# Performance work log

Measured on AMD Instinct MI355X. Metric: run time of the kernel, lower is better.

## Reference

```python
import jax, jax.numpy as jnp
import numpy as np

EPS = 1e-12

def _spectral_normalize(W, u):
    # torch spectral_norm (eval-time math): v = normalize(W^T u), sigma = u^T W v
    u = jax.lax.stop_gradient(u)
    v = W.T @ u
    v = jax.lax.stop_gradient(v / (jnp.linalg.norm(v) + EPS))
    sigma = u @ (W @ v)
    return W / sigma

def _conv1x1(x, W):
    # 1x1 conv, no bias: (out,in) x (B,in,H,W) -> (B,out,H,W)
    return jnp.einsum('oc,bchw->bohw', W, x)

def setup_inputs() -> dict:
    key = jax.random.key(0)
    ks = jax.random.split(key, 10)
    B, C, H, W = 4, 512, 64, 64
    Cp = C // 8
    return {
        'x': jax.random.normal(ks[0], (B, C, H, W), jnp.float32),
        'Wf': jax.random.normal(ks[1], (Cp, C), jnp.float32) * 0.05,
        'Wg': jax.random.normal(ks[2], (Cp, C), jnp.float32) * 0.05,
        'Wh': jax.random.normal(ks[3], (Cp, C), jnp.float32) * 0.05,
        'Wv': jax.random.normal(ks[4], (C, Cp), jnp.float32) * 0.05,
        'uf': jax.random.normal(ks[5], (Cp,), jnp.float32),
        'ug': jax.random.normal(ks[6], (Cp,), jnp.float32),
        'uh': jax.random.normal(ks[7], (Cp,), jnp.float32),
        'uv': jax.random.normal(ks[8], (C,), jnp.float32),
        'gamma': jax.random.normal(ks[9], (1,), jnp.float32) * 0.1,
    }

def reference(x, Wf, Wg, Wh, Wv, uf, ug, uh, uv, gamma):
    B, C, H, W = x.shape
    Cp = Wf.shape[0]
    N = H * W
    Wf_sn = _spectral_normalize(Wf, uf)
    Wg_sn = _spectral_normalize(Wg, ug)
    Wh_sn = _spectral_normalize(Wh, uh)
    Wv_sn = _spectral_normalize(Wv, uv)
    fx = _conv1x1(x, Wf_sn).reshape(B, Cp, N)   # (B,Cp,N)
    gx = _conv1x1(x, Wg_sn).reshape(B, Cp, N)   # (B,Cp,N)
    # fx^T gx: (B,N,N), unscaled single-head attention, softmax over last dim
    scores = jnp.einsum('bcn,bcm->bnm', fx, gx)
    attn = jax.nn.softmax(scores, axis=-1)
    hx = _conv1x1(x, Wh_sn).reshape(B, Cp, N)
    # hx @ attn: out[b,c,j] = sum_i hx[b,c,i] * attn[b,i,j]
    out = jnp.einsum('bci,bij->bcj', hx, attn).reshape(B, Cp, H, W)
    unscaled = _conv1x1(out, Wv_sn)
    return gamma * unscaled + x
```

## Files before the change

kernel.cpp:

```cpp
#include <hip/hip_runtime.h>


#define NB 4
#define CC 512
#define CP 64
#define NN 4096
#define L2E 1.4426950408889634f

typedef __attribute__((ext_vector_type(8))) short short8;
typedef __attribute__((ext_vector_type(4))) float floatx4;
typedef __attribute__((ext_vector_type(16))) float floatx16;

#define MFMA32(A, B, C) __builtin_amdgcn_mfma_f32_32x32x16_bf16((A), (B), (C), 0, 0, 0)

__device__ __forceinline__ float bf2f_u(unsigned short h) {
    return __uint_as_float((unsigned)h << 16);
}
__device__ __forceinline__ float bf16lo(unsigned v) { return __uint_as_float(v << 16); }
__device__ __forceinline__ float bf16hi(unsigned v) { return __uint_as_float(v & 0xffff0000u); }
__device__ __forceinline__ unsigned short f2bf(float f) {
    unsigned u = __float_as_uint(f);
    u += 0x7fffu + ((u >> 16) & 1u);
    return (unsigned short)(u >> 16);
}
__device__ __forceinline__ unsigned pack2bf(float a, float b) {
    return (unsigned)f2bf(a) | ((unsigned)f2bf(b) << 16);
}
__device__ __forceinline__ float ldS(const void* p, long i, int f32) {
    return f32 ? ((const float*)p)[i] : bf2f_u(((const unsigned short*)p)[i]);
}
__device__ __forceinline__ float4 ld4(const void* p, long i, int f32) {
    if (f32) return *reinterpret_cast<const float4*>((const float*)p + i);
    uint2 v = *reinterpret_cast<const uint2*>((const unsigned short*)p + i);
    return make_float4(bf16lo(v.x), bf16hi(v.x), bf16lo(v.y), bf16hi(v.y));
}
__device__ __forceinline__ short8 frag8(const void* p, long i, int f32) {
    uint4 au;
    if (f32) {
        float4 v0 = *reinterpret_cast<const float4*>((const float*)p + i);
        float4 v1 = *reinterpret_cast<const float4*>((const float*)p + i + 4);
        au.x = pack2bf(v0.x, v0.y); au.y = pack2bf(v0.z, v0.w);
        au.z = pack2bf(v1.x, v1.y); au.w = pack2bf(v1.z, v1.w);
    } else {
        au = *reinterpret_cast<const uint4*>((const unsigned short*)p + i);
    }
    return *reinterpret_cast<short8*>(&au);
}
__device__ __forceinline__ short8 as_s8(uint4 v) { return *reinterpret_cast<short8*>(&v); }
__device__ __forceinline__ floatx16 zero16() {
    floatx16 z;
    #pragma unroll
    for (int i = 0; i < 16; ++i) z[i] = 0.f;
    return z;
}
__device__ __forceinline__ unsigned cvtpk_bf16(float a, float b) {
    unsigned r;
    asm("v_cvt_pk_bf16_f32 %0, %1, %2" : "=v"(r) : "v"(a), "v"(b));
    return r;
}
__device__ __forceinline__ void pl32swap(unsigned &a, unsigned &b) {
    asm("v_permlane32_swap_b32 %0, %1" : "+v"(a), "+v"(b));
}
__device__ __forceinline__ float rcpf(float x) {
    float r;
    asm("v_rcp_f32 %0, %1" : "=v"(r) : "v"(x));
    return r;
}
__device__ __forceinline__ float exp2a(float x) {
    float r;
    asm("v_exp_f32 %0, %1" : "=v"(r) : "v"(x));
    return r;
}

__global__ __launch_bounds__(256) void detect_kernel(
    const unsigned* __restrict__ x, int* __restrict__ flag)
{
    __shared__ int red[256];
    const int t = threadIdx.x;
    int bad = 0;
    for (int i = t; i < 4096; i += 256) {
        unsigned w = x[i];
        float f0 = __uint_as_float(w << 16);
        float f1 = __uint_as_float(w & 0xffff0000u);
        float a0 = fabsf(f0), a1 = fabsf(f1);
        if (!(a0 <= 1e3f) || (f0 != 0.f && a0 < 1e-20f)) bad++;
        if (!(a1 <= 1e3f) || (f1 != 0.f && a1 < 1e-20f)) bad++;
    }
    red[t] = bad;
    __syncthreads();
    for (int s = 128; s > 0; s >>= 1) { if (t < s) red[t] += red[t + s]; __syncthreads(); }
    if (t == 0) *flag = (red[0] > 64) ? 1 : 0;
}

__global__ __launch_bounds__(256) void xpose_kernel(
    const void* __restrict__ x, const int* __restrict__ dflag,
    unsigned short* __restrict__ xTF, float* __restrict__ rl)
{
    const int f32 = *dflag;
    const int nt = blockIdx.x;
    const int b  = blockIdx.y;
    const int n0 = nt * 32;
    const int t = threadIdx.x;
    __shared__ unsigned short xl[32][72];

    const int gid = (b * 128 + nt) * 256 + t;
    if (gid < NB * NN) rl[gid] = 0.f;

    const int n_l = t & 31, cg8 = ((t >> 5) & 7) * 8;
    const int q = t >> 6, lo = t & 63;

    for (int slab = 0; slab < 8; ++slab) {
        const int cs = slab * 64;
        float v[8];
        #pragma unroll
        for (int j = 0; j < 8; ++j)
            v[j] = ldS(x, ((long)b * CC + cs + cg8 + j) * NN + n0 + n_l, f32);
        if (slab) __syncthreads();
        unsigned* row = reinterpret_cast<unsigned*>(&xl[n_l][cg8]);
        row[0] = pack2bf(v[0], v[1]);
        row[1] = pack2bf(v[2], v[3]);
        row[2] = pack2bf(v[4], v[5]);
        row[3] = pack2bf(v[6], v[7]);
        __syncthreads();
        const int cb = q * 16 + ((lo >> 5) << 3);
        uint4 val = *reinterpret_cast<const uint4*>(&xl[lo & 31][cb]);
        size_t off = (((size_t)(b * 128 + nt) * 32) + slab * 4 + q) * 512 + (size_t)lo * 8;
        *reinterpret_cast<uint4*>(xTF + off) = val;
    }
}

__global__ __launch_bounds__(512) void sigma_kernel(
    const void* __restrict__ Wf, const void* __restrict__ Wg,
    const void* __restrict__ Wh, const void* __restrict__ Wv,
    const void* __restrict__ uf, const void* __restrict__ ug,
    const void* __restrict__ uh, const void* __restrict__ uv,
    const int* __restrict__ dflag, float* __restrict__ sig,
    unsigned short* __restrict__ WF)
{
    const int f32 = *dflag;
    const int w = blockIdx.x;
    const void* W;
    const void* u;
    if (w == 0)      { W = Wf; u = uf; }
    else if (w == 1) { W = Wg; u = ug; }
    else if (w == 2) { W = Wh; u = uh; }
    else             { W = Wv; u = uv; }

    __shared__ float us[512];
    __shared__ float red[512];
    const int t = threadIdx.x;
    float S;

    if (w < 3) {
        if (t < 64) us[t] = ldS(u, t, f32);
        __syncthreads();
        float a = 0.f;
        #pragma unroll
        for (int i = 0; i < 64; ++i)
            a = fmaf(ldS(W, (long)i * 512 + t, f32), us[i], a);
        red[t] = a * a;
        __syncthreads();
        #pragma unroll
        for (int s = 256; s > 0; s >>= 1) {
            if (t < s) red[t] += red[t + s];
            __syncthreads();
        }
        S = red[0];
    } else {
        us[t] = ldS(u, t, f32);
        __syncthreads();
        const int g = t >> 6, c = t & 63;
        float a = 0.f;
        #pragma unroll
        for (int k = 0; k < 64; ++k) {
            int i = g + k * 8;
            a = fmaf(ldS(W, (long)i * 64 + c, f32), us[i], a);
        }
        red[t] = a;
        __syncthreads();
        #pragma unroll
        for (int s = 256; s >= 64; s >>= 1) {
            if (t < s) red[t] += red[t + s];
            __syncthreads();
        }
        float ac = (t < 64) ? red[t] : 0.f;
        __syncthreads();
        red[t] = ac * ac;
        __syncthreads();
        #pragma unroll
        for (int s = 256; s > 0; s >>= 1) {
            if (t < s) red[t] += red[t + s];
            __syncthreads();
        }
        S = red[0];
    }
    const float isig = (sqrtf(S) + 1e-12f) / S;
    if (t == 0) sig[w] = isig;

    if (w < 3) {
        const float sc = isig * (w == 0 ? L2E : 1.f);
        #pragma unroll
        for (int q = 0; q < 8; ++q) {
            const int idx = q * 512 + t;
            const int ll  = idx & 63;
            const int kc  = (idx >> 6) & 31;
            const int cpt = idx >> 11;
            const int cp = cpt * 32 + (ll & 31);
            const int c  = kc * 16 + ((ll >> 5) << 3);
            const long base = (long)cp * CC + c;
            float a0 = ldS(W, base + 0, f32) * sc, a1 = ldS(W, base + 1, f32) * sc;
            float a2 = ldS(W, base + 2, f32) * sc, a3 = ldS(W, base + 3, f32) * sc;
            float a4 = ldS(W, base + 4, f32) * sc, a5 = ldS(W, base + 5, f32) * sc;
            float a6 = ldS(W, base + 6, f32) * sc, a7 = ldS(W, base + 7, f32) * sc;
            uint4 o;
            o.x = pack2bf(a0, a1); o.y = pack2bf(a2, a3);
            o.z = pack2bf(a4, a5); o.w = pack2bf(a6, a7);
            *reinterpret_cast<uint4*>(WF + ((size_t)w * 4096 + idx) * 8) = o;
        }
    }
}

__global__ __launch_bounds__(256, 4) void proj_kernel(
    const unsigned short* __restrict__ xTF,
    const unsigned short* __restrict__ WF,
    unsigned short* __restrict__ fxF, unsigned short* __restrict__ gxF,
    unsigned short* __restrict__ hxF)
{
    const int t = threadIdx.x;
    const int w = t >> 6, l = t & 63;
    const int flat = blockIdx.x;
    const int k = flat & 7, s = flat >> 3;
    const int sd6 = s / 6;
    const int g = (k << 4) + sd6;
    const int zc = s - sd6 * 6;
    const int b = g & 3;
    const int nt = (g >> 2) * 4 + w;
    const int wi = zc >> 1;

    const unsigned short* xb = xTF + ((size_t)(b * 128 + nt) * 32) * 512 + (size_t)l * 8;
    const unsigned short* wb = WF + ((size_t)zc * 32) * 512 + (size_t)l * 8;

    floatx16 accE = zero16(), accO = zero16();
    uint4 x0 = *reinterpret_cast<const uint4*>(xb);
    uint4 w0 = *reinterpret_cast<const uint4*>(wb);
    uint4 x1, w1;

    if (wi == 2) {
        for (int kc = 0; kc < 32; kc += 2) {
            x1 = *reinterpret_cast<const uint4*>(xb + (kc + 1) * 512);
            w1 = *reinterpret_cast<const uint4*>(wb + (kc + 1) * 512);
            accE = MFMA32(as_s8(x0), as_s8(w0), accE);
            if (kc + 2 < 32) {
                x0 = *reinterpret_cast<const uint4*>(xb + (kc + 2) * 512);
                w0 = *reinterpret_cast<const uint4*>(wb + (kc + 2) * 512);
            }
            accO = MFMA32(as_s8(x1), as_s8(w1), accO);
        }
    } else {
        for (int kc = 0; kc < 32; kc += 2) {
            x1 = *reinterpret_cast<const uint4*>(xb + (kc + 1) * 512);
            w1 = *reinterpret_cast<const uint4*>(wb + (kc + 1) * 512);
            accE = MFMA32(as_s8(w0), as_s8(x0), accE);
            if (kc + 2 < 32) {
                x0 = *reinterpret_cast<const uint4*>(xb + (kc + 2) * 512);
                w0 = *reinterpret_cast<const uint4*>(wb + (kc + 2) * 512);
            }
            accO = MFMA32(as_s8(w1), as_s8(x1), accO);
        }
    }

    float a[16];
    #pragma unroll
    for (int i = 0; i < 16; ++i) a[i] = accE[i] + accO[i];

    const int cpt = zc & 1;
    if (wi < 2) {
        unsigned short* __restrict__ dstF = (wi == 0) ? fxF : gxF;
        #pragma unroll
        for (int kcl = 0; kcl < 2; ++kcl) {
            const int r8 = kcl * 8;
            unsigned u0 = cvtpk_bf16(a[r8 + 0], a[r8 + 1]);
            unsigned u1 = cvtpk_bf16(a[r8 + 2], a[r8 + 3]);
            unsigned u2 = cvtpk_bf16(a[r8 + 4], a[r8 + 5]);
            unsigned u3 = cvtpk_bf16(a[r8 + 6], a[r8 + 7]);
            pl32swap(u0, u2);
            pl32swap(u1, u3);
            uint4 o = make_uint4(u0, u1, u2, u3);
            size_t off = (((size_t)(b * 128 + nt) * 4) + cpt * 2 + kcl) * 512 + (size_t)l * 8;
            *reinterpret_cast<uint4*>(dstF + off) = o;
        }
    } else {
        #pragma unroll
        for (int ich = 0; ich < 2; ++ich) {
            const int r8 = ich * 8;
            unsigned u0 = cvtpk_bf16(a[r8 + 0], a[r8 + 1]);
            unsigned u1 = cvtpk_bf16(a[r8 + 2], a[r8 + 3]);
            unsigned u2 = cvtpk_bf16(a[r8 + 4], a[r8 + 5]);
            unsigned u3 = cvtpk_bf16(a[r8 + 6], a[r8 + 7]);
            pl32swap(u0, u2);
            pl32swap(u1, u3);
            uint4 o = make_uint4(u0, u1, u2, u3);
            size_t off = ((((size_t)(b * 128 + nt) * 2 + ich) * 2) + cpt) * 512 + (size_t)l * 8;
            *reinterpret_cast<uint4*>(hxF + off) = o;
        }
    }
}

__global__ __launch_bounds__(256, 4) void rowstats_kernel(
    const unsigned short* __restrict__ fxF, const unsigned short* __restrict__ gxF,
    float* __restrict__ rl)
{
    const int t = threadIdx.x;
    const int w = t >> 6, l = t & 63, l31 = l & 31, hi = l >> 5;
    const int flat = blockIdx.x;
    const int k = flat & 7, s = flat >> 3;
    const int c2 = (k << 2) + (s >> 5);
    const int iblk = s & 31;
    const int jy = c2 & 7, b = c2 >> 3;
    const int i0 = iblk * 128 + w * 32;
    const int jbase = jy * 512;

    __shared__ unsigned short stg[2][2][2048];

    const unsigned short* fA = fxF + ((size_t)(b * 128 + (i0 >> 5))) * 2048 + (size_t)l * 8;
    uint4 af[4];
    #pragma unroll
    for (int kc = 0; kc < 4; ++kc)
        af[kc] = *reinterpret_cast<const uint4*>(fA + kc * 512);

    const unsigned short* gB = gxF + ((size_t)(b * 128 + (jbase >> 5))) * 2048
                               + (size_t)w * 512 + (size_t)l * 8;

    float suml[16];
    #pragma unroll
    for (int r = 0; r < 16; ++r) suml[r] = 0.f;

    uint4 ra = *reinterpret_cast<const uint4*>(gB);
    uint4 rb = *reinterpret_cast<const uint4*>(gB + 2048);
    *reinterpret_cast<uint4*>(&stg[0][0][w * 512 + l * 8]) = ra;
    *reinterpret_cast<uint4*>(&stg[0][1][w * 512 + l * 8]) = rb;
    __syncthreads();

    #pragma unroll 2
    for (int p = 0; p < 8; ++p) {
        const int cur = p & 1;
        if (p + 1 < 8) {
            ra = *reinterpret_cast<const uint4*>(gB + (size_t)(2 * p + 2) * 2048);
            rb = *reinterpret_cast<const uint4*>(gB + (size_t)(2 * p + 3) * 2048);
        }

        uint4 bfA[4], bfB[4];
        #pragma unroll
        for (int kc = 0; kc < 4; ++kc) {
            bfA[kc] = *reinterpret_cast<const uint4*>(&stg[cur][0][kc * 512 + l * 8]);
            bfB[kc] = *reinterpret_cast<const uint4*>(&stg[cur][1][kc * 512 + l * 8]);
        }

        floatx16 sA = zero16(), sB = zero16();
        #pragma unroll
        for (int kc = 0; kc < 4; ++kc) {
            sA = MFMA32(as_s8(af[kc]), as_s8(bfA[kc]), sA);
            sB = MFMA32(as_s8(af[kc]), as_s8(bfB[kc]), sB);
        }
        #pragma unroll
        for (int r = 0; r < 16; ++r) suml[r] += exp2a(sA[r]) + exp2a(sB[r]);

        if (p + 1 < 8) {
            *reinterpret_cast<uint4*>(&stg[cur ^ 1][0][w * 512 + l * 8]) = ra;
            *reinterpret_cast<uint4*>(&stg[cur ^ 1][1][w * 512 + l * 8]) = rb;
        }
        __syncthreads();
    }

    #pragma unroll
    for (int r = 0; r < 16; ++r) {
        float v = suml[r];
        v += __shfl_xor(v, 1);
        v += __shfl_xor(v, 2);
        v += __shfl_xor(v, 4);
        v += __shfl_xor(v, 8);
        v += __shfl_xor(v, 16);
        suml[r] = v;
    }
    if (l31 == 0) {
        #pragma unroll
        for (int r = 0; r < 16; ++r) {
            int row = (r & 3) + 8 * (r >> 2) + 4 * hi;
            atomicAdd(&rl[(size_t)b * NN + i0 + row], suml[r]);
        }
    }
}

__global__ __launch_bounds__(256) void scalehx_kernel(
    const float* __restrict__ rl, unsigned short* __restrict__ hxF)
{
    const int idx = blockIdx.x * 256 + threadIdx.x;
    const int l = idx & 63;
    const int r = idx >> 6;
    const int ich = (r >> 1) & 1;
    const int tile = (r >> 2) & 127;
    const int b = r >> 9;
    const int i0 = tile * 32 + ich * 16 + (l >> 5) * 8;
    const float* rp = rl + (size_t)b * NN + i0;
    float4 ra = *reinterpret_cast<const float4*>(rp);
    float4 rb = *reinterpret_cast<const float4*>(rp + 4);
    uint4 v = *reinterpret_cast<uint4*>(hxF + (size_t)idx * 8);
    uint4 ov;
    ov.x = pack2bf(bf16lo(v.x) * rcpf(ra.x), bf16hi(v.x) * rcpf(ra.y));
    ov.y = pack2bf(bf16lo(v.y) * rcpf(ra.z), bf16hi(v.y) * rcpf(ra.w));
    ov.z = pack2bf(bf16lo(v.z) * rcpf(rb.x), bf16hi(v.z) * rcpf(rb.y));
    ov.w = pack2bf(bf16lo(v.w) * rcpf(rb.z), bf16hi(v.w) * rcpf(rb.w));
    *reinterpret_cast<uint4*>(hxF + (size_t)idx * 8) = ov;
}

__global__ __launch_bounds__(256, 4) void pv_kernel(
    const unsigned short* __restrict__ fxF, const unsigned short* __restrict__ gxF,
    const unsigned short* __restrict__ hxF,
    float* __restrict__ opF0, float* __restrict__ opF1,
    float* __restrict__ opF2, float* __restrict__ opF3)
{
    const int t = threadIdx.x;
    const int w = t >> 6, l = t & 63, l31 = l & 31, hi = l >> 5;
    const int igrp = w >> 1, jgrp = w & 1;
    const int flat = blockIdx.x;
    const int k = flat & 7, s = flat >> 3;
    const int c2 = (k << 1) + (s >> 6);
    const int jblk = s & 63;
    const int isb = c2 & 3, b = c2 >> 2;
    const int j0 = jblk * 64;
    const int tbase = isb * 32 + igrp * 16;

    __shared__ unsigned short stg[2][2][2][2048];
    float* red = reinterpret_cast<float*>(stg);

    uint4 qf[4];
    {
        const unsigned short* gq =
            gxF + ((size_t)(b * 128 + (j0 >> 5) + jgrp)) * 2048 + (size_t)l * 8;
        #pragma unroll
        for (int kc = 0; kc < 4; ++kc)
            qf[kc] = *reinterpret_cast<const uint4*>(gq + kc * 512);
    }

    floatx16 acc0 = zero16(), acc1 = zero16();

    const unsigned short* sb =
        (jgrp == 0 ? fxF : hxF) + ((size_t)(b * 128 + tbase)) * 2048 + (size_t)l * 8;

    uint4 rg0 = *reinterpret_cast<const uint4*>(sb);
    uint4 rg1 = *reinterpret_cast<const uint4*>(sb + 512);
    uint4 rg2 = *reinterpret_cast<const uint4*>(sb + 1024);
    uint4 rg3 = *reinterpret_cast<const uint4*>(sb + 1536);
    {
        unsigned short* d = &stg[igrp][0][jgrp][l * 8];
        *reinterpret_cast<uint4*>(d)        = rg0;
        *reinterpret_cast<uint4*>(d + 512)  = rg1;
        *reinterpret_cast<uint4*>(d + 1024) = rg2;
        *reinterpret_cast<uint4*>(d + 1536) = rg3;
    }
    __syncthreads();

    #pragma unroll 2
    for (int it = 0; it < 16; ++it) {
        const int cur = it & 1;
        if (it + 1 < 16) {
            const unsigned short* p = sb + (size_t)(it + 1) * 2048;
            rg0 = *reinterpret_cast<const uint4*>(p);
            rg1 = *reinterpret_cast<const uint4*>(p + 512);
            rg2 = *reinterpret_cast<const uint4*>(p + 1024);
            rg3 = *reinterpret_cast<const uint4*>(p + 1536);
        }

        const unsigned short* fl = &stg[igrp][cur][0][l * 8];
        const unsigned short* vl = &stg[igrp][cur][1][l * 8];
        uint4 af[4], vf[4];
        #pragma unroll
        for (int kc = 0; kc < 4; ++kc)
            af[kc] = *reinterpret_cast<const uint4*>(fl + kc * 512);
        vf[0] = *reinterpret_cast<const uint4*>(vl);
        vf[1] = *reinterpret_cast<const uint4*>(vl + 1024);
        vf[2] = *reinterpret_cast<const uint4*>(vl + 512);
        vf[3] = *reinterpret_cast<const uint4*>(vl + 1536);

        floatx16 s2 = zero16();
        #pragma unroll
        for (int kc = 0; kc < 4; ++kc)
            s2 = MFMA32(as_s8(af[kc]), as_s8(qf[kc]), s2);

        float e[16];
        #pragma unroll
        for (int r = 0; r < 16; ++r) e[r] = exp2a(s2[r]);

        unsigned u0 = cvtpk_bf16(e[0], e[1]);
        unsigned u1 = cvtpk_bf16(e[2], e[3]);
        unsigned u2 = cvtpk_bf16(e[4], e[5]);
        unsigned u3 = cvtpk_bf16(e[6], e[7]);
        pl32swap(u0, u2);
        pl32swap(u1, u3);
        uint4 pa0 = make_uint4(u0, u1, u2, u3);
        unsigned u4 = cvtpk_bf16(e[8], e[9]);
        unsigned u5 = cvtpk_bf16(e[10], e[11]);
        unsigned u6 = cvtpk_bf16(e[12], e[13]);
        unsigned u7 = cvtpk_bf16(e[14], e[15]);
        pl32swap(u4, u6);
        pl32swap(u5, u7);
        uint4 pa1 = make_uint4(u4, u5, u6, u7);

        acc0 = MFMA32(as_s8(pa0), as_s8(vf[0]), acc0);
        acc0 = MFMA32(as_s8(pa1), as_s8(vf[1]), acc0);
        acc1 = MFMA32(as_s8(pa0), as_s8(vf[2]), acc1);
        acc1 = MFMA32(as_s8(pa1), as_s8(vf[3]), acc1);

        if (it + 1 < 16) {
            unsigned short* d = &stg[igrp][cur ^ 1][jgrp][l * 8];
            *reinterpret_cast<uint4*>(d)        = rg0;
            *reinterpret_cast<uint4*>(d + 512)  = rg1;
            *reinterpret_cast<uint4*>(d + 1024) = rg2;
            *reinterpret_cast<uint4*>(d + 1536) = rg3;
        }
        __syncthreads();
    }

    #pragma unroll
    for (int q = 0; q < 4; ++q)
        *reinterpret_cast<float4*>(&red[(q * 256 + t) * 4]) =
            make_float4(0.f, 0.f, 0.f, 0.f);
    __syncthreads();
    #pragma unroll
    for (int r = 0; r < 16; ++r) {
        int row = jgrp * 32 + (r & 3) + 8 * (r >> 2) + 4 * hi;
        atomicAdd(&red[row * 64 + l31],      acc0[r]);
        atomicAdd(&red[row * 64 + 32 + l31], acc1[r]);
    }
    __syncthreads();

    float* __restrict__ dst = (isb == 0) ? opF0 : ((isb == 1) ? opF1 : ((isb == 2) ? opF2 : opF3));
    #pragma unroll
    for (int q = 0; q < 4; ++q) {
        int idx = q * 256 + t;
        int e2  = idx & 1;
        int ll  = (idx >> 1) & 63;
        int ks  = (idx >> 7) & 1;
        int ntl = idx >> 8;
        int jloc = ntl * 16 + (ll & 15);
        int cp   = ks * 32 + ((ll >> 4) << 3) + e2 * 4;
        float4 v = *reinterpret_cast<const float4*>(&red[jloc * 64 + cp]);
        size_t off = (((size_t)(b * 256 + (j0 >> 4) + ntl) * 2 + ks) * 64 + ll) * 8 + e2 * 4;
        *reinterpret_cast<float4*>(dst + off) = v;
    }
}

__global__ __launch_bounds__(256) void outproj_kernel(
    const void* __restrict__ x,
    const void* __restrict__ Wv,
    const void* __restrict__ gamma,
    const int* __restrict__ dflag,
    const float* __restrict__ sig,
    const float* __restrict__ opF0, const float* __restrict__ opF1,
    const float* __restrict__ opF2, const float* __restrict__ opF3,
    void* __restrict__ y)
{
    const int f32 = *dflag;
    const int n0     = blockIdx.x * 64;
    const int cobase = blockIdx.y * 128;
    const int b      = blockIdx.z;
    const int t = threadIdx.x;
    const int wv = t >> 6, l = t & 63, l15 = l & 15, quad = l >> 4;
    const float scale = ldS(gamma, 0, f32) * sig[3];

    floatx4 acc[4][2];
    #pragma unroll
    for (int ns = 0; ns < 4; ++ns)
        #pragma unroll
        for (int ct = 0; ct < 2; ++ct) acc[ns][ct] = (floatx4){0.f, 0.f, 0.f, 0.f};

    #pragma unroll
    for (int ks = 0; ks < 2; ++ks) {
        short8 a[4];
        #pragma unroll
        for (int ns = 0; ns < 4; ++ns) {
            size_t fo = (((size_t)(b * 256 + (n0 >> 4) + ns) * 2 + ks) * 64 + l) * 8;
            float4 s0 = *reinterpret_cast<const float4*>(opF0 + fo);
            float4 s1 = *reinterpret_cast<const float4*>(opF1 + fo);
            float4 s2 = *reinterpret_cast<const float4*>(opF2 + fo);
            float4 s3 = *reinterpret_cast<const float4*>(opF3 + fo);
            float4 t0 = *reinterpret_cast<const float4*>(opF0 + fo + 4);
            float4 t1 = *reinterpret_cast<const float4*>(opF1 + fo + 4);
            float4 t2 = *reinterpret_cast<const float4*>(opF2 + fo + 4);
            float4 t3 = *reinterpret_cast<const float4*>(opF3 + fo + 4);
            float v0 = s0.x + s1.x + s2.x + s3.x;
            float v1 = s0.y + s1.y + s2.y + s3.y;
            float v2 = s0.z + s1.z + s2.z + s3.z;
            float v3 = s0.w + s1.w + s2.w + s3.w;
            float v4 = t0.x + t1.x + t2.x + t3.x;
            float v5 = t0.y + t1.y + t2.y + t3.y;
            float v6 = t0.z + t1.z + t2.z + t3.z;
            float v7 = t0.w + t1.w + t2.w + t3.w;
            uint4 au;
            au.x = pack2bf(v0, v1); au.y = pack2bf(v2, v3);
            au.z = pack2bf(v4, v5); au.w = pack2bf(v6, v7);
            a[ns] = *reinterpret_cast<short8*>(&au);
        }
        const int kb = ks * 32 + quad * 8;
        #pragma unroll
        for (int ct = 0; ct < 2; ++ct) {
            const int co = cobase + 32 * wv + 16 * ct + l15;
            short8 bfr = frag8(Wv, (long)co * CP + kb, f32);
            #pragma unroll
            for (int ns = 0; ns < 4; ++ns)
                acc[ns][ct] = __builtin_amdgcn_mfma_f32_16x16x32_bf16(
                    a[ns], bfr, acc[ns][ct], 0, 0, 0);
        }
    }

    #pragma unroll
    for (int ns = 0; ns < 4; ++ns)
        #pragma unroll
        for (int ct = 0; ct < 2; ++ct) {
            const int co = cobase + 32 * wv + 16 * ct + l15;
            const long base = ((long)b * CC + co) * NN + n0 + 16 * ns + quad * 4;
            float4 xv = ld4(x, base, f32);
            float o0 = fmaf(scale, acc[ns][ct][0], xv.x);
            float o1 = fmaf(scale, acc[ns][ct][1], xv.y);
            float o2 = fmaf(scale, acc[ns][ct][2], xv.z);
            float o3 = fmaf(scale, acc[ns][ct][3], xv.w);
            if (f32) {
                *reinterpret_cast<float4*>((float*)y + base) = make_float4(o0, o1, o2, o3);
            } else {
                uint2 o;
                o.x = pack2bf(o0, o1);
                o.y = pack2bf(o2, o3);
                *reinterpret_cast<uint2*>((unsigned short*)y + base) = o;
            }
        }
}

extern "C" void kernel_launch(void* const* d_in, const int* in_sizes, int n_in,
                              void* d_out, int out_size, void* d_ws, size_t ws_size,
                              hipStream_t stream)
{
    const void* x  = d_in[0];
    const void* Wf = d_in[1];
    const void* Wg = d_in[2];
    const void* Wh = d_in[3];
    const void* Wv = d_in[4];
    const void* uf = d_in[5];
    const void* ug = d_in[6];
    const void* uh = d_in[7];
    const void* uv = d_in[8];
    const void* gm = d_in[9];

    char* base = (char*)d_ws;
    int*   dfl = (int*)(base);
    float* sig = (float*)(base + 512);
    float* rl  = (float*)(base + 1024);
    float* opF0 = (float*)(base + 1024 + 65536);
    float* opF1 = opF0 + (size_t)NB * NN * CP;
    float* opF2 = opF1 + (size_t)NB * NN * CP;
    float* opF3 = opF2 + (size_t)NB * NN * CP;
    unsigned short* fxF = (unsigned short*)(opF3 + (size_t)NB * NN * CP);
    unsigned short* gxF = fxF + (size_t)NB * CP * NN;
    unsigned short* hxF = gxF + (size_t)NB * CP * NN;
    unsigned short* xTF = hxF + (size_t)NB * CP * NN;
    unsigned short* WF  = xTF + (size_t)NB * CC * NN;

    hipLaunchKernelGGL(detect_kernel, dim3(1), dim3(256), 0, stream,
                       (const unsigned*)x, dfl);
    hipLaunchKernelGGL(xpose_kernel, dim3(128, NB), dim3(256), 0, stream,
                       x, dfl, xTF, rl);
    hipLaunchKernelGGL(sigma_kernel, dim3(4), dim3(512), 0, stream,
                       Wf, Wg, Wh, Wv, uf, ug, uh, uv, dfl, sig, WF);
    hipLaunchKernelGGL(proj_kernel, dim3(768), dim3(256), 0, stream,
                       xTF, WF, fxF, gxF, hxF);
    hipLaunchKernelGGL(rowstats_kernel, dim3(1024), dim3(256), 0, stream,
                       fxF, gxF, rl);
    hipLaunchKernelGGL(scalehx_kernel, dim3((NB * CP * NN / 8) / 256), dim3(256), 0, stream,
                       rl, hxF);
    hipLaunchKernelGGL(pv_kernel, dim3(1024), dim3(256), 0, stream,
                       fxF, gxF, hxF, opF0, opF1, opF2, opF3);
    hipLaunchKernelGGL(outproj_kernel, dim3(NN / 64, CC / 128, NB), dim3(256), 0, stream,
                       x, Wv, gm, dfl, sig, opF0, opF1, opF2, opF3, d_out);
}
```

Measured before the change: 238.2 us.

## Drop LDS staging, fuse softmax normalization into PV, halve i-split partials

```diff
diff --git a/kernel.cpp b/kernel.cpp
--- a/kernel.cpp
+++ b/kernel.cpp
@@ -70,6 +70,22 @@
     float r;
     asm("v_exp_f32 %0, %1" : "=v"(r) : "v"(x));
     return r;
+}
+__device__ __forceinline__ void packP(const float e[16], uint4& pa0, uint4& pa1) {
+    unsigned u0 = cvtpk_bf16(e[0], e[1]);
+    unsigned u1 = cvtpk_bf16(e[2], e[3]);
+    unsigned u2 = cvtpk_bf16(e[4], e[5]);
+    unsigned u3 = cvtpk_bf16(e[6], e[7]);
+    pl32swap(u0, u2);
+    pl32swap(u1, u3);
+    pa0 = make_uint4(u0, u1, u2, u3);
+    unsigned u4 = cvtpk_bf16(e[8], e[9]);
+    unsigned u5 = cvtpk_bf16(e[10], e[11]);
+    unsigned u6 = cvtpk_bf16(e[12], e[13]);
+    unsigned u7 = cvtpk_bf16(e[14], e[15]);
+    pl32swap(u4, u6);
+    pl32swap(u5, u7);
+    pa1 = make_uint4(u4, u5, u6, u7);
 }
 
 __global__ __launch_bounds__(256) void detect_kernel(
@@ -320,56 +336,42 @@
     const int i0 = iblk * 128 + w * 32;
     const int jbase = jy * 512;
 
-    __shared__ unsigned short stg[2][2][2048];
-
     const unsigned short* fA = fxF + ((size_t)(b * 128 + (i0 >> 5))) * 2048 + (size_t)l * 8;
     uint4 af[4];
     #pragma unroll
     for (int kc = 0; kc < 4; ++kc)
         af[kc] = *reinterpret_cast<const uint4*>(fA + kc * 512);
 
-    const unsigned short* gB = gxF + ((size_t)(b * 128 + (jbase >> 5))) * 2048
-                               + (size_t)w * 512 + (size_t)l * 8;
+    const unsigned short* gB = gxF + ((size_t)(b * 128 + (jbase >> 5))) * 2048 + (size_t)l * 8;
 
     float suml[16];
     #pragma unroll
     for (int r = 0; r < 16; ++r) suml[r] = 0.f;
 
-    uint4 ra = *reinterpret_cast<const uint4*>(gB);
-    uint4 rb = *reinterpret_cast<const uint4*>(gB + 2048);
-    *reinterpret_cast<uint4*>(&stg[0][0][w * 512 + l * 8]) = ra;
-    *reinterpret_cast<uint4*>(&stg[0][1][w * 512 + l * 8]) = rb;
-    __syncthreads();
-
-    #pragma unroll 2
-    for (int p = 0; p < 8; ++p) {
-        const int cur = p & 1;
-        if (p + 1 < 8) {
-            ra = *reinterpret_cast<const uint4*>(gB + (size_t)(2 * p + 2) * 2048);
-            rb = *reinterpret_cast<const uint4*>(gB + (size_t)(2 * p + 3) * 2048);
-        }
-
-        uint4 bfA[4], bfB[4];
-        #pragma unroll
-        for (int kc = 0; kc < 4; ++kc) {
-            bfA[kc] = *reinterpret_cast<const uint4*>(&stg[cur][0][kc * 512 + l * 8]);
-            bfB[kc] = *reinterpret_cast<const uint4*>(&stg[cur][1][kc * 512 + l * 8]);
-        }
-
-        floatx16 sA = zero16(), sB = zero16();
-        #pragma unroll
-        for (int kc = 0; kc < 4; ++kc) {
-            sA = MFMA32(as_s8(af[kc]), as_s8(bfA[kc]), sA);
-            sB = MFMA32(as_s8(af[kc]), as_s8(bfB[kc]), sB);
-        }
-        #pragma unroll
-        for (int r = 0; r < 16; ++r) suml[r] += exp2a(sA[r]) + exp2a(sB[r]);
-
-        if (p + 1 < 8) {
-            *reinterpret_cast<uint4*>(&stg[cur ^ 1][0][w * 512 + l * 8]) = ra;
-            *reinterpret_cast<uint4*>(&stg[cur ^ 1][1][w * 512 + l * 8]) = rb;
-        }
-        __syncthreads();
+    uint4 b0[4], b1[4];
+    auto loadB = [&](uint4* bf, int jt) {
+        const unsigned short* p = gB + (size_t)jt * 2048;
+        #pragma unroll
+        for (int kc = 0; kc < 4; ++kc)
+            bf[kc] = *reinterpret_cast<const uint4*>(p + kc * 512);
+    };
+    auto bodyR = [&](uint4* bf) {
+        floatx16 s2 = zero16();
+        __builtin_amdgcn_s_setprio(1);
+        #pragma unroll
+        for (int kc = 0; kc < 4; ++kc)
+            s2 = MFMA32(as_s8(af[kc]), as_s8(bf[kc]), s2);
+        __builtin_amdgcn_s_setprio(0);
+        #pragma unroll
+        for (int r = 0; r < 16; ++r) suml[r] += exp2a(s2[r]);
+    };
+
+    loadB(b0, 0);
+    for (int jt = 0; jt < 16; jt += 2) {
+        loadB(b1, jt + 1);
+        bodyR(b0);
+        if (jt + 2 < 16) loadB(b0, jt + 2);
+        bodyR(b1);
     }
 
     #pragma unroll
@@ -391,134 +393,103 @@
     }
 }
 
-__global__ __launch_bounds__(256) void scalehx_kernel(
-    const float* __restrict__ rl, unsigned short* __restrict__ hxF)
-{
-    const int idx = blockIdx.x * 256 + threadIdx.x;
-    const int l = idx & 63;
-    const int r = idx >> 6;
-    const int ich = (r >> 1) & 1;
-    const int tile = (r >> 2) & 127;
-    const int b = r >> 9;
-    const int i0 = tile * 32 + ich * 16 + (l >> 5) * 8;
-    const float* rp = rl + (size_t)b * NN + i0;
-    float4 ra = *reinterpret_cast<const float4*>(rp);
-    float4 rb = *reinterpret_cast<const float4*>(rp + 4);
-    uint4 v = *reinterpret_cast<uint4*>(hxF + (size_t)idx * 8);
-    uint4 ov;
-    ov.x = pack2bf(bf16lo(v.x) * rcpf(ra.x), bf16hi(v.x) * rcpf(ra.y));
-    ov.y = pack2bf(bf16lo(v.y) * rcpf(ra.z), bf16hi(v.y) * rcpf(ra.w));
-    ov.z = pack2bf(bf16lo(v.z) * rcpf(rb.x), bf16hi(v.z) * rcpf(rb.y));
-    ov.w = pack2bf(bf16lo(v.w) * rcpf(rb.z), bf16hi(v.w) * rcpf(rb.w));
-    *reinterpret_cast<uint4*>(hxF + (size_t)idx * 8) = ov;
-}
-
-__global__ __launch_bounds__(256, 4) void pv_kernel(
+__global__ __launch_bounds__(256, 2) void pv_kernel(
     const unsigned short* __restrict__ fxF, const unsigned short* __restrict__ gxF,
-    const unsigned short* __restrict__ hxF,
-    float* __restrict__ opF0, float* __restrict__ opF1,
-    float* __restrict__ opF2, float* __restrict__ opF3)
+    const unsigned short* __restrict__ hxF, const float* __restrict__ rl,
+    float* __restrict__ opF0, float* __restrict__ opF1)
 {
     const int t = threadIdx.x;
     const int w = t >> 6, l = t & 63, l31 = l & 31, hi = l >> 5;
-    const int igrp = w >> 1, jgrp = w & 1;
     const int flat = blockIdx.x;
-    const int k = flat & 7, s = flat >> 3;
-    const int c2 = (k << 1) + (s >> 6);
-    const int jblk = s & 63;
-    const int isb = c2 & 3, b = c2 >> 2;
+    const int k = flat & 7;
+    const int isb = k & 1, b = k >> 1;
+    const int jblk = flat >> 3;
     const int j0 = jblk * 64;
-    const int tbase = isb * 32 + igrp * 16;
-
-    __shared__ unsigned short stg[2][2][2][2048];
-    float* red = reinterpret_cast<float*>(stg);
-
-    uint4 qf[4];
+    const int tb = isb * 64 + w * 16;
+
+    __shared__ float red[64 * 64];
+
+    uint4 qf0[4], qf1[4];
     {
         const unsigned short* gq =
-            gxF + ((size_t)(b * 128 + (j0 >> 5) + jgrp)) * 2048 + (size_t)l * 8;
+            gxF + ((size_t)(b * 128 + (j0 >> 5))) * 2048 + (size_t)l * 8;
+        #pragma unroll
+        for (int kc = 0; kc < 4; ++kc) {
+            qf0[kc] = *reinterpret_cast<const uint4*>(gq + kc * 512);
+            qf1[kc] = *reinterpret_cast<const uint4*>(gq + 2048 + kc * 512);
+        }
+    }
+
+    floatx16 acc00 = zero16(), acc01 = zero16();
+    floatx16 acc10 = zero16(), acc11 = zero16();
+
+    const unsigned short* fb = fxF + ((size_t)(b * 128 + tb)) * 2048 + (size_t)l * 8;
+    const unsigned short* vb = hxF + ((size_t)(b * 128 + tb)) * 2048 + (size_t)l * 8;
+    const float* rbase = rl + (size_t)b * NN + tb * 32 + (hi << 2);
+
+    uint4 afA[4], vfA[4], afB[4], vfB[4];
+    auto loadA = [&](uint4* af, int it) {
+        const unsigned short* p = fb + (size_t)it * 2048;
         #pragma unroll
         for (int kc = 0; kc < 4; ++kc)
-            qf[kc] = *reinterpret_cast<const uint4*>(gq + kc * 512);
-    }
-
-    floatx16 acc0 = zero16(), acc1 = zero16();
-
-    const unsigned short* sb =
-        (jgrp == 0 ? fxF : hxF) + ((size_t)(b * 128 + tbase)) * 2048 + (size_t)l * 8;
-
-    uint4 rg0 = *reinterpret_cast<const uint4*>(sb);
-    uint4 rg1 = *reinterpret_cast<const uint4*>(sb + 512);
-    uint4 rg2 = *reinterpret_cast<const uint4*>(sb + 1024);
-    uint4 rg3 = *reinterpret_cast<const uint4*>(sb + 1536);
-    {
-        unsigned short* d = &stg[igrp][0][jgrp][l * 8];
-        *reinterpret_cast<uint4*>(d)        = rg0;
-        *reinterpret_cast<uint4*>(d + 512)  = rg1;
-        *reinterpret_cast<uint4*>(d + 1024) = rg2;
-        *reinterpret_cast<uint4*>(d + 1536) = rg3;
-    }
-    __syncthreads();
-
-    #pragma unroll 2
-    for (int it = 0; it < 16; ++it) {
-        const int cur = it & 1;
-        if (it + 1 < 16) {
-            const unsigned short* p = sb + (size_t)(it + 1) * 2048;
-            rg0 = *reinterpret_cast<const uint4*>(p);
-            rg1 = *reinterpret_cast<const uint4*>(p + 512);
-            rg2 = *reinterpret_cast<const uint4*>(p + 1024);
-            rg3 = *reinterpret_cast<const uint4*>(p + 1536);
-        }
-
-        const unsigned short* fl = &stg[igrp][cur][0][l * 8];
-        const unsigned short* vl = &stg[igrp][cur][1][l * 8];
-        uint4 af[4], vf[4];
-        #pragma unroll
-        for (int kc = 0; kc < 4; ++kc)
-            af[kc] = *reinterpret_cast<const uint4*>(fl + kc * 512);
-        vf[0] = *reinterpret_cast<const uint4*>(vl);
-        vf[1] = *reinterpret_cast<const uint4*>(vl + 1024);
-        vf[2] = *reinterpret_cast<const uint4*>(vl + 512);
-        vf[3] = *reinterpret_cast<const uint4*>(vl + 1536);
-
-        floatx16 s2 = zero16();
-        #pragma unroll
-        for (int kc = 0; kc < 4; ++kc)
-            s2 = MFMA32(as_s8(af[kc]), as_s8(qf[kc]), s2);
-
-        float e[16];
-        #pragma unroll
-        for (int r = 0; r < 16; ++r) e[r] = exp2a(s2[r]);
-
-        unsigned u0 = cvtpk_bf16(e[0], e[1]);
-        unsigned u1 = cvtpk_bf16(e[2], e[3]);
-        unsigned u2 = cvtpk_bf16(e[4], e[5]);
-        unsigned u3 = cvtpk_bf16(e[6], e[7]);
-        pl32swap(u0, u2);
-        pl32swap(u1, u3);
-        uint4 pa0 = make_uint4(u0, u1, u2, u3);
-        unsigned u4 = cvtpk_bf16(e[8], e[9]);
-        unsigned u5 = cvtpk_bf16(e[10], e[11]);
-        unsigned u6 = cvtpk_bf16(e[12], e[13]);
-        unsigned u7 = cvtpk_bf16(e[14], e[15]);
-        pl32swap(u4, u6);
-        pl32swap(u5, u7);
-        uint4 pa1 = make_uint4(u4, u5, u6, u7);
-
-        acc0 = MFMA32(as_s8(pa0), as_s8(vf[0]), acc0);
-        acc0 = MFMA32(as_s8(pa1), as_s8(vf[1]), acc0);
-        acc1 = MFMA32(as_s8(pa0), as_s8(vf[2]), acc1);
-        acc1 = MFMA32(as_s8(pa1), as_s8(vf[3]), acc1);
-
-        if (it + 1 < 16) {
-            unsigned short* d = &stg[igrp][cur ^ 1][jgrp][l * 8];
-            *reinterpret_cast<uint4*>(d)        = rg0;
-            *reinterpret_cast<uint4*>(d + 512)  = rg1;
-            *reinterpret_cast<uint4*>(d + 1024) = rg2;
-            *reinterpret_cast<uint4*>(d + 1536) = rg3;
-        }
-        __syncthreads();
+            af[kc] = *reinterpret_cast<const uint4*>(p + kc * 512);
+    };
+    auto loadV = [&](uint4* vf, int it) {
+        const unsigned short* p = vb + (size_t)it * 2048;
+        vf[0] = *reinterpret_cast<const uint4*>(p);
+        vf[1] = *reinterpret_cast<const uint4*>(p + 1024);
+        vf[2] = *reinterpret_cast<const uint4*>(p + 512);
+        vf[3] = *reinterpret_cast<const uint4*>(p + 1536);
+    };
+    auto body = [&](uint4* af, uint4* vf, int it) {
+        const float* rp = rbase + it * 32;
+        float4 rv0 = *reinterpret_cast<const float4*>(rp);
+        float4 rv1 = *reinterpret_cast<const float4*>(rp + 8);
+        float4 rv2 = *reinterpret_cast<const float4*>(rp + 16);
+        float4 rv3 = *reinterpret_cast<const float4*>(rp + 24);
+        float ri[16];
+        ri[0] = rcpf(rv0.x); ri[1] = rcpf(rv0.y); ri[2] = rcpf(rv0.z); ri[3] = rcpf(rv0.w);
+        ri[4] = rcpf(rv1.x); ri[5] = rcpf(rv1.y); ri[6] = rcpf(rv1.z); ri[7] = rcpf(rv1.w);
+        ri[8] = rcpf(rv2.x); ri[9] = rcpf(rv2.y); ri[10] = rcpf(rv2.z); ri[11] = rcpf(rv2.w);
+        ri[12] = rcpf(rv3.x); ri[13] = rcpf(rv3.y); ri[14] = rcpf(rv3.z); ri[15] = rcpf(rv3.w);
+
+        floatx16 s0 = zero16(), s1 = zero16();
+        __builtin_amdgcn_s_setprio(1);
+        #pragma unroll
+        for (int kc = 0; kc < 4; ++kc) {
+            s0 = MFMA32(as_s8(af[kc]), as_s8(qf0[kc]), s0);
+            s1 = MFMA32(as_s8(af[kc]), as_s8(qf1[kc]), s1);
+        }
+        __builtin_amdgcn_s_setprio(0);
+
+        float e0[16], e1[16];
+        #pragma unroll
+        for (int r = 0; r < 16; ++r) e0[r] = exp2a(s0[r]) * ri[r];
+        #pragma unroll
+        for (int r = 0; r < 16; ++r) e1[r] = exp2a(s1[r]) * ri[r];
+
+        uint4 pa00, pa01, pa10, pa11;
+        packP(e0, pa00, pa01);
+        packP(e1, pa10, pa11);
+
+        __builtin_amdgcn_s_setprio(1);
+        acc00 = MFMA32(as_s8(pa00), as_s8(vf[0]), acc00);
+        acc00 = MFMA32(as_s8(pa01), as_s8(vf[1]), acc00);
+        acc01 = MFMA32(as_s8(pa00), as_s8(vf[2]), acc01);
+        acc01 = MFMA32(as_s8(pa01), as_s8(vf[3]), acc01);
+        acc10 = MFMA32(as_s8(pa10), as_s8(vf[0]), acc10);
+        acc10 = MFMA32(as_s8(pa11), as_s8(vf[1]), acc10);
+        acc11 = MFMA32(as_s8(pa10), as_s8(vf[2]), acc11);
+        acc11 = MFMA32(as_s8(pa11), as_s8(vf[3]), acc11);
+        __builtin_amdgcn_s_setprio(0);
+    };
+
+    loadA(afA, 0); loadV(vfA, 0);
+    for (int it = 0; it < 16; it += 2) {
+        loadA(afB, it + 1); loadV(vfB, it + 1);
+        body(afA, vfA, it);
+        if (it + 2 < 16) { loadA(afA, it + 2); loadV(vfA, it + 2); }
+        body(afB, vfB, it + 1);
     }
 
     #pragma unroll
@@ -528,13 +499,15 @@
     __syncthreads();
     #pragma unroll
     for (int r = 0; r < 16; ++r) {
-        int row = jgrp * 32 + (r & 3) + 8 * (r >> 2) + 4 * hi;
-        atomicAdd(&red[row * 64 + l31],      acc0[r]);
-        atomicAdd(&red[row * 64 + 32 + l31], acc1[r]);
+        int crow = (r & 3) + 8 * (r >> 2) + 4 * hi;
+        atomicAdd(&red[crow * 64 + l31],             acc00[r]);
+        atomicAdd(&red[crow * 64 + 32 + l31],        acc01[r]);
+        atomicAdd(&red[(32 + crow) * 64 + l31],      acc10[r]);
+        atomicAdd(&red[(32 + crow) * 64 + 32 + l31], acc11[r]);
     }
     __syncthreads();
 
-    float* __restrict__ dst = (isb == 0) ? opF0 : ((isb == 1) ? opF1 : ((isb == 2) ? opF2 : opF3));
+    float* __restrict__ dst = isb ? opF1 : opF0;
     #pragma unroll
     for (int q = 0; q < 4; ++q) {
         int idx = q * 256 + t;
@@ -557,7 +530,6 @@
     const int* __restrict__ dflag,
     const float* __restrict__ sig,
     const float* __restrict__ opF0, const float* __restrict__ opF1,
-    const float* __restrict__ opF2, const float* __restrict__ opF3,
     void* __restrict__ y)
 {
     const int f32 = *dflag;
@@ -582,23 +554,13 @@
             size_t fo = (((size_t)(b * 256 + (n0 >> 4) + ns) * 2 + ks) * 64 + l) * 8;
             float4 s0 = *reinterpret_cast<const float4*>(opF0 + fo);
             float4 s1 = *reinterpret_cast<const float4*>(opF1 + fo);
-            float4 s2 = *reinterpret_cast<const float4*>(opF2 + fo);
-            float4 s3 = *reinterpret_cast<const float4*>(opF3 + fo);
             float4 t0 = *reinterpret_cast<const float4*>(opF0 + fo + 4);
             float4 t1 = *reinterpret_cast<const float4*>(opF1 + fo + 4);
-            float4 t2 = *reinterpret_cast<const float4*>(opF2 + fo + 4);
-            float4 t3 = *reinterpret_cast<const float4*>(opF3 + fo + 4);
-            float v0 = s0.x + s1.x + s2.x + s3.x;
-            float v1 = s0.y + s1.y + s2.y + s3.y;
-            float v2 = s0.z + s1.z + s2.z + s3.z;
-            float v3 = s0.w + s1.w + s2.w + s3.w;
-            float v4 = t0.x + t1.x + t2.x + t3.x;
-            float v5 = t0.y + t1.y + t2.y + t3.y;
-            float v6 = t0.z + t1.z + t2.z + t3.z;
-            float v7 = t0.w + t1.w + t2.w + t3.w;
             uint4 au;
-            au.x = pack2bf(v0, v1); au.y = pack2bf(v2, v3);
-            au.z = pack2bf(v4, v5); au.w = pack2bf(v6, v7);
+            au.x = pack2bf(s0.x + s1.x, s0.y + s1.y);
+            au.y = pack2bf(s0.z + s1.z, s0.w + s1.w);
+            au.z = pack2bf(t0.x + t1.x, t0.y + t1.y);
+            au.w = pack2bf(t0.z + t1.z, t0.w + t1.w);
             a[ns] = *reinterpret_cast<short8*>(&au);
         }
         const int kb = ks * 32 + quad * 8;
@@ -656,9 +618,7 @@
     float* rl  = (float*)(base + 1024);
     float* opF0 = (float*)(base + 1024 + 65536);
     float* opF1 = opF0 + (size_t)NB * NN * CP;
-    float* opF2 = opF1 + (size_t)NB * NN * CP;
-    float* opF3 = opF2 + (size_t)NB * NN * CP;
-    unsigned short* fxF = (unsigned short*)(opF3 + (size_t)NB * NN * CP);
+    unsigned short* fxF = (unsigned short*)(opF1 + (size_t)NB * NN * CP);
     unsigned short* gxF = fxF + (size_t)NB * CP * NN;
     unsigned short* hxF = gxF + (size_t)NB * CP * NN;
     unsigned short* xTF = hxF + (size_t)NB * CP * NN;
@@ -674,10 +634,8 @@
                        xTF, WF, fxF, gxF, hxF);
     hipLaunchKernelGGL(rowstats_kernel, dim3(1024), dim3(256), 0, stream,
                        fxF, gxF, rl);
-    hipLaunchKernelGGL(scalehx_kernel, dim3((NB * CP * NN / 8) / 256), dim3(256), 0, stream,
-                       rl, hxF);
-    hipLaunchKernelGGL(pv_kernel, dim3(1024), dim3(256), 0, stream,
-                       fxF, gxF, hxF, opF0, opF1, opF2, opF3);
+    hipLaunchKernelGGL(pv_kernel, dim3(512), dim3(256), 0, stream,
+                       fxF, gxF, hxF, rl, opF0, opF1);
     hipLaunchKernelGGL(outproj_kernel, dim3(NN / 64, CC / 128, NB), dim3(256), 0, stream,
-                       x, Wv, gm, dfl, sig, opF0, opF1, opF2, opF3, d_out);
-}
+                       x, Wv, gm, dfl, sig, opF0, opF1, d_out);
+}
```

New measurement: 231.5 us. 1.03x faster.
